# Kernel tuning notes

Measured on AMD Instinct MI355X. Metric: run time of the kernel, lower is better.

The kernel has to match this reference:

```python
import jax, jax.numpy as jnp
import numpy as np

EPS = 1e-8  # torch.nn.CosineSimilarity default eps

def setup_inputs() -> dict:
    key = jax.random.key(0)
    k1, k2 = jax.random.split(key)
    B, R, T, D = 256, 36, 64, 1024
    img_feats = jax.random.normal(k1, (B, R, D), dtype=jnp.float32)
    cap_feats = jax.random.normal(k2, (B, T, D), dtype=jnp.float32)
    cap_mask = jnp.ones((B, T), dtype=jnp.float32)  # unused by the original forward
    return {"img_feats": img_feats, "cap_feats": cap_feats, "cap_mask": cap_mask}

def reference(img_feats, cap_feats, cap_mask):
    # img_feats: (B, R, D); cap_feats: (B, T, D)
    # cosine similarity between every region r and every caption word t:
    # scores[b, r, t] = (img[b,r] . cap[b,t]) / max(||img[b,r]|| * ||cap[b,t]||, eps)
    dots = jnp.einsum('brd,btd->brt', img_feats, cap_feats)
    img_norm = jnp.linalg.norm(img_feats, axis=-1)  # (B, R)
    cap_norm = jnp.linalg.norm(cap_feats, axis=-1)  # (B, T)
    denom = jnp.maximum(img_norm[:, :, None] * cap_norm[:, None, :], EPS)
    scores = dots / denom  # (B, R, T)
    # softmax over regions (dim=1 in the original)
    attn = jax.nn.softmax(scores, axis=1)  # (B, R, T)
    # weighted sum over regions -> per-word image representation (B, T, D)
    img_cap_reps = jnp.einsum('brt,brd->btd', attn, img_feats)
    return img_cap_reps
```

## Files before the change

### kernel.cpp

```cpp
#include <hip/hip_runtime.h>

#define RREG 36
#define TTOK 64
#define DDIM 1024

typedef __attribute__((ext_vector_type(4))) float f32x4;
typedef __attribute__((ext_vector_type(8))) short bf16x8;

__device__ __forceinline__ unsigned short f2bf(float x) {
  unsigned int u = __float_as_uint(x);
  u += 0x7fffu + ((u >> 16) & 1u);
  return (unsigned short)(u >> 16);
}

__global__ __launch_bounds__(1024) void scan_fused(
    const float* __restrict__ img, const float* __restrict__ cap,
    float* __restrict__ out) {
  __shared__ __align__(16) unsigned char smem[52032];

  unsigned short* scap  = (unsigned short*)(smem + 0);
  unsigned short* simg  = (unsigned short*)(smem + 17408);
  unsigned short* simgT = (unsigned short*)(smem + 0);
  float* ssc            = (float*)(smem + 32768);
  unsigned short* satt  = (unsigned short*)(smem + 45440);
  float* sni            = (float*)(smem + 51584);
  float* snc            = (float*)(smem + 51776);

  const int tid  = threadIdx.x;
  const int lane = tid & 63;
  const int wave = tid >> 6;
  const int fm   = lane & 15;
  const int kq   = lane >> 4;
  const int b    = blockIdx.x;

  const float* imgb = img + (size_t)b * RREG * DDIM;
  const float* capb = cap + (size_t)b * TTOK * DDIM;
  float*       outb = out + (size_t)b * TTOK * DDIM;

  const int mt = wave >> 2;
  const int nt = wave & 3;

  f32x4 acc = {0.f, 0.f, 0.f, 0.f};
  float cn0 = 0.f, cn1 = 0.f, in0 = 0.f, in1 = 0.f;

  const int trow = tid >> 5;
  const int d4   = tid & 31;

  for (int c = 0; c < 8; ++c) {
    const int dbase = c * 128 + d4 * 4;
    {
      float4 v = *(const float4*)(capb + trow * DDIM + dbase);
      cn0 += v.x * v.x + v.y * v.y + v.z * v.z + v.w * v.w;
      ushort4 p; p.x = f2bf(v.x); p.y = f2bf(v.y); p.z = f2bf(v.z); p.w = f2bf(v.w);
      *(ushort4*)(scap + trow * 136 + d4 * 4) = p;

      float4 w = *(const float4*)(capb + (trow + 32) * DDIM + dbase);
      cn1 += w.x * w.x + w.y * w.y + w.z * w.z + w.w * w.w;
      ushort4 q; q.x = f2bf(w.x); q.y = f2bf(w.y); q.z = f2bf(w.z); q.w = f2bf(w.w);
      *(ushort4*)(scap + (trow + 32) * 136 + d4 * 4) = q;
    }
    {
      float4 v = *(const float4*)(imgb + trow * DDIM + dbase);
      in0 += v.x * v.x + v.y * v.y + v.z * v.z + v.w * v.w;
      ushort4 p; p.x = f2bf(v.x); p.y = f2bf(v.y); p.z = f2bf(v.z); p.w = f2bf(v.w);
      *(ushort4*)(simg + trow * 136 + d4 * 4) = p;
      if (tid < 512) {
        int r2 = trow + 32;
        float4 w = make_float4(0.f, 0.f, 0.f, 0.f);
        if (r2 < RREG) {
          w = *(const float4*)(imgb + r2 * DDIM + dbase);
          in1 += w.x * w.x + w.y * w.y + w.z * w.z + w.w * w.w;
        }
        ushort4 q; q.x = f2bf(w.x); q.y = f2bf(w.y); q.z = f2bf(w.z); q.w = f2bf(w.w);
        *(ushort4*)(simg + r2 * 136 + d4 * 4) = q;
      }
    }
    __syncthreads();
    if (wave < 12) {
      const unsigned short* arow = simg + (mt * 16 + fm) * 136 + kq * 8;
      const unsigned short* brow = scap + (nt * 16 + fm) * 136 + kq * 8;
#pragma unroll
      for (int ks = 0; ks < 4; ++ks) {
        bf16x8 av = *(const bf16x8*)(arow + ks * 32);
        bf16x8 bv = *(const bf16x8*)(brow + ks * 32);
        acc = __builtin_amdgcn_mfma_f32_16x16x32_bf16(av, bv, acc, 0, 0, 0);
      }
    }
    __syncthreads();
  }

  if (wave < 12) {
#pragma unroll
    for (int i = 0; i < 4; ++i)
      ssc[(mt * 16 + kq * 4 + i) * 66 + nt * 16 + fm] = acc[i];
  }
#pragma unroll
  for (int off = 16; off > 0; off >>= 1) {
    cn0 += __shfl_down(cn0, off, 32);
    cn1 += __shfl_down(cn1, off, 32);
    in0 += __shfl_down(in0, off, 32);
    in1 += __shfl_down(in1, off, 32);
  }
  if ((tid & 31) == 0) {
    snc[trow]      = sqrtf(cn0);
    snc[trow + 32] = sqrtf(cn1);
    sni[trow]      = sqrtf(in0);
    if (trow < 16) sni[trow + 32] = sqrtf(in1);
  }
  __syncthreads();

  if (wave == 0) {
    float cn = snc[lane];
    float s[RREG];
    float mx = -1e30f;
#pragma unroll
    for (int r = 0; r < RREG; ++r) {
      float denom = fmaxf(sni[r] * cn, 1e-8f);
      float v = ssc[r * 66 + lane] / denom;
      s[r] = v;
      mx = fmaxf(mx, v);
    }
    float sum = 0.f;
#pragma unroll
    for (int r = 0; r < RREG; ++r) { float e = __expf(s[r] - mx); s[r] = e; sum += e; }
    float rinv = 1.f / sum;
    unsigned short* ap = satt + lane * 48;
#pragma unroll
    for (int r = 0; r < RREG; ++r) ap[r] = f2bf(s[r] * rinv);
#pragma unroll
    for (int r = RREG; r < 48; ++r) ap[r] = 0;
  }
  __syncthreads();

  const int mtB = wave >> 2;
  const unsigned short* arowB = satt + (mtB * 16 + fm) * 48;
  bf16x8 a1 = *(const bf16x8*)(arowB + kq * 8);
  bf16x8 a2 = {0, 0, 0, 0, 0, 0, 0, 0};
  if (kq < 2) a2 = *(const bf16x8*)(arowB + 32 + kq * 8);

  for (int cb = 0; cb < 8; ++cb) {
    __syncthreads();
    for (int f = tid; f < 1536; f += 1024) {
      int g = f & 511;
      int r = (f >> 9) * 16 + (g & 15);
      int qd = (g >> 4) & 3;
      int sd = g >> 6;
      int dloc = (qd + 4 * sd) * 4;
      float4 v = make_float4(0.f, 0.f, 0.f, 0.f);
      if (r < RREG) v = *(const float4*)(imgb + r * DDIM + cb * 128 + dloc);
      simgT[(dloc + 0) * 56 + r] = f2bf(v.x);
      simgT[(dloc + 1) * 56 + r] = f2bf(v.y);
      simgT[(dloc + 2) * 56 + r] = f2bf(v.z);
      simgT[(dloc + 3) * 56 + r] = f2bf(v.w);
    }
    __syncthreads();
#pragma unroll
    for (int j = 0; j < 2; ++j) {
      int ntB = (wave & 3) * 2 + j;
      const unsigned short* brow = simgT + (ntB * 16 + fm) * 56;
      bf16x8 b1 = *(const bf16x8*)(brow + kq * 8);
      bf16x8 b2 = {0, 0, 0, 0, 0, 0, 0, 0};
      if (kq < 2) b2 = *(const bf16x8*)(brow + 32 + kq * 8);
      f32x4 o = {0.f, 0.f, 0.f, 0.f};
      o = __builtin_amdgcn_mfma_f32_16x16x32_bf16(a1, b1, o, 0, 0, 0);
      o = __builtin_amdgcn_mfma_f32_16x16x32_bf16(a2, b2, o, 0, 0, 0);
#pragma unroll
      for (int i = 0; i < 4; ++i)
        outb[(mtB * 16 + kq * 4 + i) * DDIM + cb * 128 + ntB * 16 + fm] = o[i];
    }
  }
}

extern "C" void kernel_launch(void* const* d_in, const int* in_sizes, int n_in,
                              void* d_out, int out_size, void* d_ws, size_t ws_size,
                              hipStream_t stream) {
  const float* img = (const float*)d_in[0];
  const float* cap = (const float*)d_in[1];
  float* out = (float*)d_out;
  scan_fused<<<dim3(256), dim3(1024), 0, stream>>>(img, cap, out);
}
```

Measured before the change: 159.0 us.

## Split tokens across two blocks and register-prefetch global loads

Each batch now spans two 512-thread blocks, each handling 32 caption tokens, so the grid grows from 256 to 512 blocks and uses smaller LDS for higher occupancy. Both the score GEMM and the weighted-sum loops prefetch the next chunk's global loads into registers before converting and storing the current chunk, which overlaps memory latency with compute. Barriers become a lightweight lgkmcnt wait plus s_barrier, and the block index is swizzled to a different batch/half mapping. The cost is that each image tile is loaded and its norms computed twice, once per token half.

```diff
diff --git a/kernel.cpp b/kernel.cpp
--- a/kernel.cpp
+++ b/kernel.cpp
@@ -3,6 +3,7 @@
 #define RREG 36
 #define TTOK 64
 #define DDIM 1024
+#define TH   32
 
 typedef __attribute__((ext_vector_type(4))) float f32x4;
 typedef __attribute__((ext_vector_type(8))) short bf16x8;
@@ -13,70 +14,95 @@
   return (unsigned short)(u >> 16);
 }
 
-__global__ __launch_bounds__(1024) void scan_fused(
+__device__ __forceinline__ void lds_barrier() {
+  asm volatile("s_waitcnt lgkmcnt(0)" ::: "memory");
+  __builtin_amdgcn_s_barrier();
+}
+
+__global__ __launch_bounds__(512, 4) void scan_fused(
     const float* __restrict__ img, const float* __restrict__ cap,
     float* __restrict__ out) {
-  __shared__ __align__(16) unsigned char smem[52032];
+  __shared__ __align__(16) unsigned char smem[31680];
 
   unsigned short* scap  = (unsigned short*)(smem + 0);
-  unsigned short* simg  = (unsigned short*)(smem + 17408);
+  unsigned short* simg  = (unsigned short*)(smem + 8704);
   unsigned short* simgT = (unsigned short*)(smem + 0);
-  float* ssc            = (float*)(smem + 32768);
-  unsigned short* satt  = (unsigned short*)(smem + 45440);
-  float* sni            = (float*)(smem + 51584);
-  float* snc            = (float*)(smem + 51776);
+  float* ssc            = (float*)(smem + 21760);
+  unsigned short* satt  = (unsigned short*)(smem + 28288);
+  float* sni            = (float*)(smem + 31360);
+  float* snc            = (float*)(smem + 31552);
 
   const int tid  = threadIdx.x;
   const int lane = tid & 63;
   const int wave = tid >> 6;
   const int fm   = lane & 15;
   const int kq   = lane >> 4;
-  const int b    = blockIdx.x;
+
+  const int i     = blockIdx.x;
+  const int b     = ((i & 7) << 5) + (i >> 4);
+  const int tbase = ((i >> 3) & 1) * TH;
 
   const float* imgb = img + (size_t)b * RREG * DDIM;
-  const float* capb = cap + (size_t)b * TTOK * DDIM;
-  float*       outb = out + (size_t)b * TTOK * DDIM;
-
-  const int mt = wave >> 2;
-  const int nt = wave & 3;
-
-  f32x4 acc = {0.f, 0.f, 0.f, 0.f};
-  float cn0 = 0.f, cn1 = 0.f, in0 = 0.f, in1 = 0.f;
+  const float* capb = cap + ((size_t)b * TTOK + tbase) * DDIM;
+  float*       outb = out + ((size_t)b * TTOK + tbase) * DDIM;
 
   const int trow = tid >> 5;
   const int d4   = tid & 31;
 
+  const int mt = wave >> 1;
+  const int nt = wave & 1;
+
+  f32x4 acc = {0.f, 0.f, 0.f, 0.f};
+  float cn0 = 0.f, cn1 = 0.f, in0 = 0.f, in1 = 0.f, in2 = 0.f;
+
+  float4 pc0, pc1, pi0, pi1, pi2;
+  {
+    const float* cp = capb + d4 * 4;
+    const float* ip = imgb + d4 * 4;
+    pc0 = *(const float4*)(cp + trow * DDIM);
+    pc1 = *(const float4*)(cp + (trow + 16) * DDIM);
+    pi0 = *(const float4*)(ip + trow * DDIM);
+    pi1 = *(const float4*)(ip + (trow + 16) * DDIM);
+    pi2 = make_float4(0.f, 0.f, 0.f, 0.f);
+    if (trow < RREG - 32) pi2 = *(const float4*)(ip + (trow + 32) * DDIM);
+  }
+
+#pragma unroll
   for (int c = 0; c < 8; ++c) {
-    const int dbase = c * 128 + d4 * 4;
+    float4 nc0, nc1, ni0, ni1, ni2;
+    if (c < 7) {
+      const float* cp = capb + (c + 1) * 128 + d4 * 4;
+      const float* ip = imgb + (c + 1) * 128 + d4 * 4;
+      nc0 = *(const float4*)(cp + trow * DDIM);
+      nc1 = *(const float4*)(cp + (trow + 16) * DDIM);
+      ni0 = *(const float4*)(ip + trow * DDIM);
+      ni1 = *(const float4*)(ip + (trow + 16) * DDIM);
+      ni2 = make_float4(0.f, 0.f, 0.f, 0.f);
+      if (trow < RREG - 32) ni2 = *(const float4*)(ip + (trow + 32) * DDIM);
+    }
     {
-      float4 v = *(const float4*)(capb + trow * DDIM + dbase);
-      cn0 += v.x * v.x + v.y * v.y + v.z * v.z + v.w * v.w;
-      ushort4 p; p.x = f2bf(v.x); p.y = f2bf(v.y); p.z = f2bf(v.z); p.w = f2bf(v.w);
+      cn0 += pc0.x * pc0.x + pc0.y * pc0.y + pc0.z * pc0.z + pc0.w * pc0.w;
+      ushort4 p; p.x = f2bf(pc0.x); p.y = f2bf(pc0.y); p.z = f2bf(pc0.z); p.w = f2bf(pc0.w);
       *(ushort4*)(scap + trow * 136 + d4 * 4) = p;
 
-      float4 w = *(const float4*)(capb + (trow + 32) * DDIM + dbase);
-      cn1 += w.x * w.x + w.y * w.y + w.z * w.z + w.w * w.w;
-      ushort4 q; q.x = f2bf(w.x); q.y = f2bf(w.y); q.z = f2bf(w.z); q.w = f2bf(w.w);
-      *(ushort4*)(scap + (trow + 32) * 136 + d4 * 4) = q;
-    }
-    {
-      float4 v = *(const float4*)(imgb + trow * DDIM + dbase);
-      in0 += v.x * v.x + v.y * v.y + v.z * v.z + v.w * v.w;
-      ushort4 p; p.x = f2bf(v.x); p.y = f2bf(v.y); p.z = f2bf(v.z); p.w = f2bf(v.w);
-      *(ushort4*)(simg + trow * 136 + d4 * 4) = p;
-      if (tid < 512) {
-        int r2 = trow + 32;
-        float4 w = make_float4(0.f, 0.f, 0.f, 0.f);
-        if (r2 < RREG) {
-          w = *(const float4*)(imgb + r2 * DDIM + dbase);
-          in1 += w.x * w.x + w.y * w.y + w.z * w.z + w.w * w.w;
-        }
-        ushort4 q; q.x = f2bf(w.x); q.y = f2bf(w.y); q.z = f2bf(w.z); q.w = f2bf(w.w);
-        *(ushort4*)(simg + r2 * 136 + d4 * 4) = q;
-      }
-    }
-    __syncthreads();
-    if (wave < 12) {
+      cn1 += pc1.x * pc1.x + pc1.y * pc1.y + pc1.z * pc1.z + pc1.w * pc1.w;
+      ushort4 q; q.x = f2bf(pc1.x); q.y = f2bf(pc1.y); q.z = f2bf(pc1.z); q.w = f2bf(pc1.w);
+      *(ushort4*)(scap + (trow + 16) * 136 + d4 * 4) = q;
+
+      in0 += pi0.x * pi0.x + pi0.y * pi0.y + pi0.z * pi0.z + pi0.w * pi0.w;
+      ushort4 r0; r0.x = f2bf(pi0.x); r0.y = f2bf(pi0.y); r0.z = f2bf(pi0.z); r0.w = f2bf(pi0.w);
+      *(ushort4*)(simg + trow * 136 + d4 * 4) = r0;
+
+      in1 += pi1.x * pi1.x + pi1.y * pi1.y + pi1.z * pi1.z + pi1.w * pi1.w;
+      ushort4 r1; r1.x = f2bf(pi1.x); r1.y = f2bf(pi1.y); r1.z = f2bf(pi1.z); r1.w = f2bf(pi1.w);
+      *(ushort4*)(simg + (trow + 16) * 136 + d4 * 4) = r1;
+
+      in2 += pi2.x * pi2.x + pi2.y * pi2.y + pi2.z * pi2.z + pi2.w * pi2.w;
+      ushort4 r2; r2.x = f2bf(pi2.x); r2.y = f2bf(pi2.y); r2.z = f2bf(pi2.z); r2.w = f2bf(pi2.w);
+      *(ushort4*)(simg + (trow + 32) * 136 + d4 * 4) = r2;
+    }
+    lds_barrier();
+    if (wave < 6) {
       const unsigned short* arow = simg + (mt * 16 + fm) * 136 + kq * 8;
       const unsigned short* brow = scap + (nt * 16 + fm) * 136 + kq * 8;
 #pragma unroll
@@ -86,13 +112,14 @@
         acc = __builtin_amdgcn_mfma_f32_16x16x32_bf16(av, bv, acc, 0, 0, 0);
       }
     }
-    __syncthreads();
-  }
-
-  if (wave < 12) {
-#pragma unroll
-    for (int i = 0; i < 4; ++i)
-      ssc[(mt * 16 + kq * 4 + i) * 66 + nt * 16 + fm] = acc[i];
+    lds_barrier();
+    if (c < 7) { pc0 = nc0; pc1 = nc1; pi0 = ni0; pi1 = ni1; pi2 = ni2; }
+  }
+
+  if (wave < 6) {
+#pragma unroll
+    for (int ii = 0; ii < 4; ++ii)
+      ssc[(mt * 16 + kq * 4 + ii) * 34 + nt * 16 + fm] = acc[ii];
   }
 #pragma unroll
   for (int off = 16; off > 0; off >>= 1) {
@@ -100,23 +127,25 @@
     cn1 += __shfl_down(cn1, off, 32);
     in0 += __shfl_down(in0, off, 32);
     in1 += __shfl_down(in1, off, 32);
+    in2 += __shfl_down(in2, off, 32);
   }
   if ((tid & 31) == 0) {
     snc[trow]      = sqrtf(cn0);
-    snc[trow + 32] = sqrtf(cn1);
+    snc[trow + 16] = sqrtf(cn1);
     sni[trow]      = sqrtf(in0);
-    if (trow < 16) sni[trow + 32] = sqrtf(in1);
-  }
-  __syncthreads();
-
-  if (wave == 0) {
+    sni[trow + 16] = sqrtf(in1);
+    if (trow < RREG - 32) sni[trow + 32] = sqrtf(in2);
+  }
+  lds_barrier();
+
+  if (wave == 0 && lane < TH) {
     float cn = snc[lane];
     float s[RREG];
     float mx = -1e30f;
 #pragma unroll
     for (int r = 0; r < RREG; ++r) {
       float denom = fmaxf(sni[r] * cn, 1e-8f);
-      float v = ssc[r * 66 + lane] / denom;
+      float v = ssc[r * 34 + lane] / denom;
       s[r] = v;
       mx = fmaxf(mx, v);
     }
@@ -130,7 +159,7 @@
 #pragma unroll
     for (int r = RREG; r < 48; ++r) ap[r] = 0;
   }
-  __syncthreads();
+  lds_barrier();
 
   const int mtB = wave >> 2;
   const unsigned short* arowB = satt + (mtB * 16 + fm) * 48;
@@ -138,25 +167,47 @@
   bf16x8 a2 = {0, 0, 0, 0, 0, 0, 0, 0};
   if (kq < 2) a2 = *(const bf16x8*)(arowB + 32 + kq * 8);
 
+  const int rB0  = tid & 15;
+  const int dloc = (((tid >> 4) & 3) + 4 * (tid >> 6)) * 4;
+
+  float4 q0, q1, q2;
+  {
+    const float* ip = imgb + dloc;
+    q0 = *(const float4*)(ip + rB0 * DDIM);
+    q1 = *(const float4*)(ip + (rB0 + 16) * DDIM);
+    q2 = make_float4(0.f, 0.f, 0.f, 0.f);
+    if (rB0 + 32 < RREG) q2 = *(const float4*)(ip + (rB0 + 32) * DDIM);
+  }
+
+#pragma unroll
   for (int cb = 0; cb < 8; ++cb) {
-    __syncthreads();
-    for (int f = tid; f < 1536; f += 1024) {
-      int g = f & 511;
-      int r = (f >> 9) * 16 + (g & 15);
-      int qd = (g >> 4) & 3;
-      int sd = g >> 6;
-      int dloc = (qd + 4 * sd) * 4;
-      float4 v = make_float4(0.f, 0.f, 0.f, 0.f);
-      if (r < RREG) v = *(const float4*)(imgb + r * DDIM + cb * 128 + dloc);
-      simgT[(dloc + 0) * 56 + r] = f2bf(v.x);
-      simgT[(dloc + 1) * 56 + r] = f2bf(v.y);
-      simgT[(dloc + 2) * 56 + r] = f2bf(v.z);
-      simgT[(dloc + 3) * 56 + r] = f2bf(v.w);
-    }
-    __syncthreads();
+    float4 n0, n1, n2;
+    if (cb < 7) {
+      const float* ip = imgb + (cb + 1) * 128 + dloc;
+      n0 = *(const float4*)(ip + rB0 * DDIM);
+      n1 = *(const float4*)(ip + (rB0 + 16) * DDIM);
+      n2 = make_float4(0.f, 0.f, 0.f, 0.f);
+      if (rB0 + 32 < RREG) n2 = *(const float4*)(ip + (rB0 + 32) * DDIM);
+    }
+    {
+      unsigned short* tp = simgT + dloc * 56;
+      tp[0 * 56 + rB0] = f2bf(q0.x);
+      tp[1 * 56 + rB0] = f2bf(q0.y);
+      tp[2 * 56 + rB0] = f2bf(q0.z);
+      tp[3 * 56 + rB0] = f2bf(q0.w);
+      tp[0 * 56 + rB0 + 16] = f2bf(q1.x);
+      tp[1 * 56 + rB0 + 16] = f2bf(q1.y);
+      tp[2 * 56 + rB0 + 16] = f2bf(q1.z);
+      tp[3 * 56 + rB0 + 16] = f2bf(q1.w);
+      tp[0 * 56 + rB0 + 32] = f2bf(q2.x);
+      tp[1 * 56 + rB0 + 32] = f2bf(q2.y);
+      tp[2 * 56 + rB0 + 32] = f2bf(q2.z);
+      tp[3 * 56 + rB0 + 32] = f2bf(q2.w);
+    }
+    lds_barrier();
 #pragma unroll
     for (int j = 0; j < 2; ++j) {
-      int ntB = (wave & 3) * 2 + j;
+      const int ntB = (wave & 3) * 2 + j;
       const unsigned short* brow = simgT + (ntB * 16 + fm) * 56;
       bf16x8 b1 = *(const bf16x8*)(brow + kq * 8);
       bf16x8 b2 = {0, 0, 0, 0, 0, 0, 0, 0};
@@ -165,8 +216,12 @@
       o = __builtin_amdgcn_mfma_f32_16x16x32_bf16(a1, b1, o, 0, 0, 0);
       o = __builtin_amdgcn_mfma_f32_16x16x32_bf16(a2, b2, o, 0, 0, 0);
 #pragma unroll
-      for (int i = 0; i < 4; ++i)
-        outb[(mtB * 16 + kq * 4 + i) * DDIM + cb * 128 + ntB * 16 + fm] = o[i];
+      for (int ii = 0; ii < 4; ++ii)
+        outb[(mtB * 16 + kq * 4 + ii) * DDIM + cb * 128 + ntB * 16 + fm] = o[ii];
+    }
+    if (cb < 7) {
+      lds_barrier();
+      q0 = n0; q1 = n1; q2 = n2;
     }
   }
 }
@@ -177,5 +232,5 @@
   const float* img = (const float*)d_in[0];
   const float* cap = (const float*)d_in[1];
   float* out = (float*)d_out;
-  scan_fused<<<dim3(256), dim3(1024), 0, stream>>>(img, cap, out);
-}
+  scan_fused<<<dim3(512), dim3(512), 0, stream>>>(img, cap, out);
+}
```

After: 200.1 us. +25.8%, slower.

## Double-buffer LDS staging with register prefetch across both GEMM phases

Applied to the files above, without the earlier changes.

Turns both GEMM phases into a software pipeline. Global loads for chunk c+2 are issued ahead while chunk c+1 is converted into the other LDS buffer and chunk c is consumed by MFMA, so each iteration needs one barrier instead of two. The first image-transpose chunks for phase two are prefetched during the tail of phase one. Barriers become a bare s_waitcnt lgkmcnt plus s_barrier, and launch bounds add a min-blocks hint. This costs more LDS and more live registers, which may hurt occupancy at 1024 threads.

```diff
diff --git a/kernel.cpp b/kernel.cpp
--- a/kernel.cpp
+++ b/kernel.cpp
@@ -13,18 +13,20 @@
   return (unsigned short)(u >> 16);
 }
 
-__global__ __launch_bounds__(1024) void scan_fused(
+__device__ __forceinline__ void lds_barrier() {
+  asm volatile("s_waitcnt lgkmcnt(0)" ::: "memory");
+  __builtin_amdgcn_s_barrier();
+}
+
+__global__ __launch_bounds__(1024, 4) void scan_fused(
     const float* __restrict__ img, const float* __restrict__ cap,
     float* __restrict__ out) {
-  __shared__ __align__(16) unsigned char smem[52032];
-
-  unsigned short* scap  = (unsigned short*)(smem + 0);
-  unsigned short* simg  = (unsigned short*)(smem + 17408);
-  unsigned short* simgT = (unsigned short*)(smem + 0);
-  float* ssc            = (float*)(smem + 32768);
-  unsigned short* satt  = (unsigned short*)(smem + 45440);
-  float* sni            = (float*)(smem + 51584);
-  float* snc            = (float*)(smem + 51776);
+  __shared__ __align__(16) unsigned char smem[60928];
+
+  float* ssc            = (float*)(smem + 30464);
+  unsigned short* satt  = (unsigned short*)(smem + 43136);
+  float* sni            = (float*)(smem + 49280);
+  float* snc            = (float*)(smem + 49472);
 
   const int tid  = threadIdx.x;
   const int lane = tid & 63;
@@ -37,48 +39,55 @@
   const float* capb = cap + (size_t)b * TTOK * DDIM;
   float*       outb = out + (size_t)b * TTOK * DDIM;
 
-  const int mt = wave >> 2;
-  const int nt = wave & 3;
+  const int trow = tid >> 5;
+  const int d4   = tid & 31;
+  const int mt   = wave >> 2;
+  const int nt   = wave & 3;
+
+  const int rB   = ((tid >> 9) << 4) | (tid & 15);
+  const int gB   = tid & 511;
+  const int dlB  = ((((gB >> 4) & 3) + ((gB >> 6) << 2)) << 2);
+  const bool hasB2 = (tid < 512);
+  const int rB2  = 32 + (tid & 15);
 
   f32x4 acc = {0.f, 0.f, 0.f, 0.f};
   float cn0 = 0.f, cn1 = 0.f, in0 = 0.f, in1 = 0.f;
 
-  const int trow = tid >> 5;
-  const int d4   = tid & 31;
-
-  for (int c = 0; c < 8; ++c) {
-    const int dbase = c * 128 + d4 * 4;
-    {
-      float4 v = *(const float4*)(capb + trow * DDIM + dbase);
-      cn0 += v.x * v.x + v.y * v.y + v.z * v.z + v.w * v.w;
-      ushort4 p; p.x = f2bf(v.x); p.y = f2bf(v.y); p.z = f2bf(v.z); p.w = f2bf(v.w);
-      *(ushort4*)(scap + trow * 136 + d4 * 4) = p;
-
-      float4 w = *(const float4*)(capb + (trow + 32) * DDIM + dbase);
-      cn1 += w.x * w.x + w.y * w.y + w.z * w.z + w.w * w.w;
-      ushort4 q; q.x = f2bf(w.x); q.y = f2bf(w.y); q.z = f2bf(w.z); q.w = f2bf(w.w);
-      *(ushort4*)(scap + (trow + 32) * 136 + d4 * 4) = q;
-    }
-    {
-      float4 v = *(const float4*)(imgb + trow * DDIM + dbase);
-      in0 += v.x * v.x + v.y * v.y + v.z * v.z + v.w * v.w;
-      ushort4 p; p.x = f2bf(v.x); p.y = f2bf(v.y); p.z = f2bf(v.z); p.w = f2bf(v.w);
-      *(ushort4*)(simg + trow * 136 + d4 * 4) = p;
-      if (tid < 512) {
-        int r2 = trow + 32;
-        float4 w = make_float4(0.f, 0.f, 0.f, 0.f);
-        if (r2 < RREG) {
-          w = *(const float4*)(imgb + r2 * DDIM + dbase);
-          in1 += w.x * w.x + w.y * w.y + w.z * w.z + w.w * w.w;
-        }
-        ushort4 q; q.x = f2bf(w.x); q.y = f2bf(w.y); q.z = f2bf(w.z); q.w = f2bf(w.w);
-        *(ushort4*)(simg + r2 * 136 + d4 * 4) = q;
-      }
-    }
-    __syncthreads();
+  auto issueA = [&](int c, float4& c0v, float4& c1v, float4& i0v, float4& i1v) {
+    const float* cp = capb + c * 128 + d4 * 4;
+    const float* ip = imgb + c * 128 + d4 * 4;
+    c0v = *(const float4*)(cp + trow * DDIM);
+    c1v = *(const float4*)(cp + (trow + 32) * DDIM);
+    i0v = *(const float4*)(ip + trow * DDIM);
+    i1v = make_float4(0.f, 0.f, 0.f, 0.f);
+    if (tid < 512 && trow + 32 < RREG)
+      i1v = *(const float4*)(ip + (trow + 32) * DDIM);
+  };
+  auto stageA = [&](int par, const float4& c0v, const float4& c1v,
+                    const float4& i0v, const float4& i1v) {
+    unsigned short* sc = (unsigned short*)(smem + par * 30464);
+    unsigned short* si = sc + 8704;
+    cn0 += c0v.x * c0v.x + c0v.y * c0v.y + c0v.z * c0v.z + c0v.w * c0v.w;
+    ushort4 p; p.x = f2bf(c0v.x); p.y = f2bf(c0v.y); p.z = f2bf(c0v.z); p.w = f2bf(c0v.w);
+    *(ushort4*)(sc + trow * 136 + d4 * 4) = p;
+    cn1 += c1v.x * c1v.x + c1v.y * c1v.y + c1v.z * c1v.z + c1v.w * c1v.w;
+    ushort4 q; q.x = f2bf(c1v.x); q.y = f2bf(c1v.y); q.z = f2bf(c1v.z); q.w = f2bf(c1v.w);
+    *(ushort4*)(sc + (trow + 32) * 136 + d4 * 4) = q;
+    in0 += i0v.x * i0v.x + i0v.y * i0v.y + i0v.z * i0v.z + i0v.w * i0v.w;
+    ushort4 r0; r0.x = f2bf(i0v.x); r0.y = f2bf(i0v.y); r0.z = f2bf(i0v.z); r0.w = f2bf(i0v.w);
+    *(ushort4*)(si + trow * 136 + d4 * 4) = r0;
+    if (tid < 512) {
+      in1 += i1v.x * i1v.x + i1v.y * i1v.y + i1v.z * i1v.z + i1v.w * i1v.w;
+      ushort4 r1; r1.x = f2bf(i1v.x); r1.y = f2bf(i1v.y); r1.z = f2bf(i1v.z); r1.w = f2bf(i1v.w);
+      *(ushort4*)(si + (trow + 32) * 136 + d4 * 4) = r1;
+    }
+  };
+  auto mfmaA = [&](int par) {
     if (wave < 12) {
-      const unsigned short* arow = simg + (mt * 16 + fm) * 136 + kq * 8;
-      const unsigned short* brow = scap + (nt * 16 + fm) * 136 + kq * 8;
+      const unsigned short* sc = (const unsigned short*)(smem + par * 30464);
+      const unsigned short* si = sc + 8704;
+      const unsigned short* arow = si + (mt * 16 + fm) * 136 + kq * 8;
+      const unsigned short* brow = sc + (nt * 16 + fm) * 136 + kq * 8;
 #pragma unroll
       for (int ks = 0; ks < 4; ++ks) {
         bf16x8 av = *(const bf16x8*)(arow + ks * 32);
@@ -86,13 +95,52 @@
         acc = __builtin_amdgcn_mfma_f32_16x16x32_bf16(av, bv, acc, 0, 0, 0);
       }
     }
-    __syncthreads();
+  };
+  auto issueB = [&](int cb, float4& q0, float4& q1) {
+    const float* ip = imgb + cb * 128 + dlB;
+    q0 = *(const float4*)(ip + rB * DDIM);
+    q1 = make_float4(0.f, 0.f, 0.f, 0.f);
+    if (hasB2 && rB2 < RREG) q1 = *(const float4*)(ip + rB2 * DDIM);
+  };
+  auto stageB = [&](int par, const float4& q0, const float4& q1) {
+    unsigned short* tp = (unsigned short*)(smem + par * 14336) + dlB * 56;
+    tp[0 * 56 + rB] = f2bf(q0.x);
+    tp[1 * 56 + rB] = f2bf(q0.y);
+    tp[2 * 56 + rB] = f2bf(q0.z);
+    tp[3 * 56 + rB] = f2bf(q0.w);
+    if (hasB2) {
+      tp[0 * 56 + rB2] = f2bf(q1.x);
+      tp[1 * 56 + rB2] = f2bf(q1.y);
+      tp[2 * 56 + rB2] = f2bf(q1.z);
+      tp[3 * 56 + rB2] = f2bf(q1.w);
+    }
+  };
+
+  float4 tc0, tc1, ti0, ti1;
+  float4 cc0, cc1, ci0, ci1;
+  float4 nc0, nc1, ni0, ni1;
+  float4 bq0a, bq0b, bq1a, bq1b;
+
+  issueA(0, tc0, tc1, ti0, ti1);
+  issueA(1, cc0, cc1, ci0, ci1);
+  stageA(0, tc0, tc1, ti0, ti1);
+  lds_barrier();
+
+  for (int c = 0; c < 8; ++c) {
+    if (c < 6)        issueA(c + 2, nc0, nc1, ni0, ni1);
+    else if (c == 6)  issueB(0, bq0a, bq0b);
+    else              issueB(1, bq1a, bq1b);
+    if (c < 7)        stageA((c + 1) & 1, cc0, cc1, ci0, ci1);
+    else              stageB(0, bq0a, bq0b);
+    mfmaA(c & 1);
+    lds_barrier();
+    cc0 = nc0; cc1 = nc1; ci0 = ni0; ci1 = ni1;
   }
 
   if (wave < 12) {
 #pragma unroll
-    for (int i = 0; i < 4; ++i)
-      ssc[(mt * 16 + kq * 4 + i) * 66 + nt * 16 + fm] = acc[i];
+    for (int i2 = 0; i2 < 4; ++i2)
+      ssc[(mt * 16 + kq * 4 + i2) * 66 + nt * 16 + fm] = acc[i2];
   }
 #pragma unroll
   for (int off = 16; off > 0; off >>= 1) {
@@ -107,7 +155,7 @@
     sni[trow]      = sqrtf(in0);
     if (trow < 16) sni[trow + 32] = sqrtf(in1);
   }
-  __syncthreads();
+  lds_barrier();
 
   if (wave == 0) {
     float cn = snc[lane];
@@ -130,7 +178,7 @@
 #pragma unroll
     for (int r = RREG; r < 48; ++r) ap[r] = 0;
   }
-  __syncthreads();
+  lds_barrier();
 
   const int mtB = wave >> 2;
   const unsigned short* arowB = satt + (mtB * 16 + fm) * 48;
@@ -138,36 +186,31 @@
   bf16x8 a2 = {0, 0, 0, 0, 0, 0, 0, 0};
   if (kq < 2) a2 = *(const bf16x8*)(arowB + 32 + kq * 8);
 
+  float4 pq0 = bq1a, pq1 = bq1b;
+  float4 nq0, nq1;
+
   for (int cb = 0; cb < 8; ++cb) {
-    __syncthreads();
-    for (int f = tid; f < 1536; f += 1024) {
-      int g = f & 511;
-      int r = (f >> 9) * 16 + (g & 15);
-      int qd = (g >> 4) & 3;
-      int sd = g >> 6;
-      int dloc = (qd + 4 * sd) * 4;
-      float4 v = make_float4(0.f, 0.f, 0.f, 0.f);
-      if (r < RREG) v = *(const float4*)(imgb + r * DDIM + cb * 128 + dloc);
-      simgT[(dloc + 0) * 56 + r] = f2bf(v.x);
-      simgT[(dloc + 1) * 56 + r] = f2bf(v.y);
-      simgT[(dloc + 2) * 56 + r] = f2bf(v.z);
-      simgT[(dloc + 3) * 56 + r] = f2bf(v.w);
-    }
-    __syncthreads();
-#pragma unroll
-    for (int j = 0; j < 2; ++j) {
-      int ntB = (wave & 3) * 2 + j;
-      const unsigned short* brow = simgT + (ntB * 16 + fm) * 56;
-      bf16x8 b1 = *(const bf16x8*)(brow + kq * 8);
-      bf16x8 b2 = {0, 0, 0, 0, 0, 0, 0, 0};
-      if (kq < 2) b2 = *(const bf16x8*)(brow + 32 + kq * 8);
-      f32x4 o = {0.f, 0.f, 0.f, 0.f};
-      o = __builtin_amdgcn_mfma_f32_16x16x32_bf16(a1, b1, o, 0, 0, 0);
-      o = __builtin_amdgcn_mfma_f32_16x16x32_bf16(a2, b2, o, 0, 0, 0);
-#pragma unroll
-      for (int i = 0; i < 4; ++i)
-        outb[(mtB * 16 + kq * 4 + i) * DDIM + cb * 128 + ntB * 16 + fm] = o[i];
-    }
+    if (cb < 6) issueB(cb + 2, nq0, nq1);
+    if (cb < 7) stageB((cb + 1) & 1, pq0, pq1);
+    {
+      const unsigned short* st = (const unsigned short*)(smem + (cb & 1) * 14336);
+#pragma unroll
+      for (int j = 0; j < 2; ++j) {
+        const int ntB = (wave & 3) * 2 + j;
+        const unsigned short* brow = st + (ntB * 16 + fm) * 56;
+        bf16x8 b1 = *(const bf16x8*)(brow + kq * 8);
+        bf16x8 b2 = {0, 0, 0, 0, 0, 0, 0, 0};
+        if (kq < 2) b2 = *(const bf16x8*)(brow + 32 + kq * 8);
+        f32x4 o = {0.f, 0.f, 0.f, 0.f};
+        o = __builtin_amdgcn_mfma_f32_16x16x32_bf16(a1, b1, o, 0, 0, 0);
+        o = __builtin_amdgcn_mfma_f32_16x16x32_bf16(a2, b2, o, 0, 0, 0);
+#pragma unroll
+        for (int i2 = 0; i2 < 4; ++i2)
+          outb[(mtB * 16 + kq * 4 + i2) * DDIM + cb * 128 + ntB * 16 + fm] = o[i2];
+      }
+    }
+    lds_barrier();
+    pq0 = nq0; pq1 = nq1;
   }
 }
 
```

Measured after the change: 163.1 us. 1.03x slower.

## Load GEMM operands directly from global into registers, dropping LDS staging

Applied to the files above, without the earlier changes.

Both matrix-multiply phases now read their MFMA operand fragments straight from global memory into registers and convert them to bf16 in place. This removes the shared-memory staging buffers and the block-wide barriers inside each chunk loop. Norms are computed from the same register loads and reduced with cross-lane shuffles. The trade is redundant global reads (each image and caption row is fetched by several waves) and strided, less coalesced column loads in the second GEMM, in exchange for much lower LDS use and less synchronisation. The launch-bounds hint is also raised to request more resident blocks.

```diff
diff --git a/kernel.cpp b/kernel.cpp
--- a/kernel.cpp
+++ b/kernel.cpp
@@ -13,18 +13,22 @@
   return (unsigned short)(u >> 16);
 }
 
-__global__ __launch_bounds__(1024) void scan_fused(
+__device__ __forceinline__ bf16x8 cvt8(float4 a, float4 b) {
+  bf16x8 r;
+  r[0] = (short)f2bf(a.x); r[1] = (short)f2bf(a.y);
+  r[2] = (short)f2bf(a.z); r[3] = (short)f2bf(a.w);
+  r[4] = (short)f2bf(b.x); r[5] = (short)f2bf(b.y);
+  r[6] = (short)f2bf(b.z); r[7] = (short)f2bf(b.w);
+  return r;
+}
+
+__global__ __launch_bounds__(1024, 4) void scan_fused(
     const float* __restrict__ img, const float* __restrict__ cap,
     float* __restrict__ out) {
-  __shared__ __align__(16) unsigned char smem[52032];
-
-  unsigned short* scap  = (unsigned short*)(smem + 0);
-  unsigned short* simg  = (unsigned short*)(smem + 17408);
-  unsigned short* simgT = (unsigned short*)(smem + 0);
-  float* ssc            = (float*)(smem + 32768);
-  unsigned short* satt  = (unsigned short*)(smem + 45440);
-  float* sni            = (float*)(smem + 51584);
-  float* snc            = (float*)(smem + 51776);
+  __shared__ __align__(16) float ssc[48 * 66];
+  __shared__ __align__(16) unsigned short satt[64 * 48];
+  __shared__ float sni[48];
+  __shared__ float snc[TTOK];
 
   const int tid  = threadIdx.x;
   const int lane = tid & 63;
@@ -37,75 +41,51 @@
   const float* capb = cap + (size_t)b * TTOK * DDIM;
   float*       outb = out + (size_t)b * TTOK * DDIM;
 
-  const int mt = wave >> 2;
-  const int nt = wave & 3;
+  if (wave < 12) {
+    const int mt = wave >> 2;
+    const int nt = wave & 3;
+    const int ar = mt * 16 + fm;
+    const int br = nt * 16 + fm;
+    const bool avld = (ar < RREG);
+    const float* ap = imgb + (size_t)ar * DDIM + kq * 8;
+    const float* bp = capb + (size_t)br * DDIM + kq * 8;
 
-  f32x4 acc = {0.f, 0.f, 0.f, 0.f};
-  float cn0 = 0.f, cn1 = 0.f, in0 = 0.f, in1 = 0.f;
+    f32x4 acc = {0.f, 0.f, 0.f, 0.f};
+    float nI = 0.f, nC = 0.f;
+    const float4 z4 = make_float4(0.f, 0.f, 0.f, 0.f);
 
-  const int trow = tid >> 5;
-  const int d4   = tid & 31;
-
-  for (int c = 0; c < 8; ++c) {
-    const int dbase = c * 128 + d4 * 4;
-    {
-      float4 v = *(const float4*)(capb + trow * DDIM + dbase);
-      cn0 += v.x * v.x + v.y * v.y + v.z * v.z + v.w * v.w;
-      ushort4 p; p.x = f2bf(v.x); p.y = f2bf(v.y); p.z = f2bf(v.z); p.w = f2bf(v.w);
-      *(ushort4*)(scap + trow * 136 + d4 * 4) = p;
-
-      float4 w = *(const float4*)(capb + (trow + 32) * DDIM + dbase);
-      cn1 += w.x * w.x + w.y * w.y + w.z * w.z + w.w * w.w;
-      ushort4 q; q.x = f2bf(w.x); q.y = f2bf(w.y); q.z = f2bf(w.z); q.w = f2bf(w.w);
-      *(ushort4*)(scap + (trow + 32) * 136 + d4 * 4) = q;
-    }
-    {
-      float4 v = *(const float4*)(imgb + trow * DDIM + dbase);
-      in0 += v.x * v.x + v.y * v.y + v.z * v.z + v.w * v.w;
-      ushort4 p; p.x = f2bf(v.x); p.y = f2bf(v.y); p.z = f2bf(v.z); p.w = f2bf(v.w);
-      *(ushort4*)(simg + trow * 136 + d4 * 4) = p;
-      if (tid < 512) {
-        int r2 = trow + 32;
-        float4 w = make_float4(0.f, 0.f, 0.f, 0.f);
-        if (r2 < RREG) {
-          w = *(const float4*)(imgb + r2 * DDIM + dbase);
-          in1 += w.x * w.x + w.y * w.y + w.z * w.z + w.w * w.w;
-        }
-        ushort4 q; q.x = f2bf(w.x); q.y = f2bf(w.y); q.z = f2bf(w.z); q.w = f2bf(w.w);
-        *(ushort4*)(simg + r2 * 136 + d4 * 4) = q;
+    for (int c = 0; c < 8; ++c) {
+      float4 A0[4], A1[4], B0[4], B1[4];
+#pragma unroll
+      for (int ks = 0; ks < 4; ++ks) {
+        const float* a = ap + c * 128 + ks * 32;
+        const float* q = bp + c * 128 + ks * 32;
+        A0[ks] = avld ? *(const float4*)(a)     : z4;
+        A1[ks] = avld ? *(const float4*)(a + 4) : z4;
+        B0[ks] = *(const float4*)(q);
+        B1[ks] = *(const float4*)(q + 4);
+      }
+#pragma unroll
+      for (int ks = 0; ks < 4; ++ks) {
+        nI += A0[ks].x * A0[ks].x + A0[ks].y * A0[ks].y +
+              A0[ks].z * A0[ks].z + A0[ks].w * A0[ks].w +
+              A1[ks].x * A1[ks].x + A1[ks].y * A1[ks].y +
+              A1[ks].z * A1[ks].z + A1[ks].w * A1[ks].w;
+        nC += B0[ks].x * B0[ks].x + B0[ks].y * B0[ks].y +
+              B0[ks].z * B0[ks].z + B0[ks].w * B0[ks].w +
+              B1[ks].x * B1[ks].x + B1[ks].y * B1[ks].y +
+              B1[ks].z * B1[ks].z + B1[ks].w * B1[ks].w;
+        acc = __builtin_amdgcn_mfma_f32_16x16x32_bf16(
+            cvt8(A0[ks], A1[ks]), cvt8(B0[ks], B1[ks]), acc, 0, 0, 0);
       }
     }
-    __syncthreads();
-    if (wave < 12) {
-      const unsigned short* arow = simg + (mt * 16 + fm) * 136 + kq * 8;
-      const unsigned short* brow = scap + (nt * 16 + fm) * 136 + kq * 8;
-#pragma unroll
-      for (int ks = 0; ks < 4; ++ks) {
-        bf16x8 av = *(const bf16x8*)(arow + ks * 32);
-        bf16x8 bv = *(const bf16x8*)(brow + ks * 32);
-        acc = __builtin_amdgcn_mfma_f32_16x16x32_bf16(av, bv, acc, 0, 0, 0);
-      }
-    }
-    __syncthreads();
-  }
-
-  if (wave < 12) {
 #pragma unroll
     for (int i = 0; i < 4; ++i)
       ssc[(mt * 16 + kq * 4 + i) * 66 + nt * 16 + fm] = acc[i];
-  }
-#pragma unroll
-  for (int off = 16; off > 0; off >>= 1) {
-    cn0 += __shfl_down(cn0, off, 32);
-    cn1 += __shfl_down(cn1, off, 32);
-    in0 += __shfl_down(in0, off, 32);
-    in1 += __shfl_down(in1, off, 32);
-  }
-  if ((tid & 31) == 0) {
-    snc[trow]      = sqrtf(cn0);
-    snc[trow + 32] = sqrtf(cn1);
-    sni[trow]      = sqrtf(in0);
-    if (trow < 16) sni[trow + 32] = sqrtf(in1);
+    nI += __shfl_xor(nI, 16); nI += __shfl_xor(nI, 32);
+    nC += __shfl_xor(nC, 16); nC += __shfl_xor(nC, 32);
+    if (nt == 0 && kq == 0 && avld) sni[ar] = sqrtf(nI);
+    if (mt == 0 && kq == 0)         snc[br] = sqrtf(nC);
   }
   __syncthreads();
 
@@ -124,11 +104,11 @@
 #pragma unroll
     for (int r = 0; r < RREG; ++r) { float e = __expf(s[r] - mx); s[r] = e; sum += e; }
     float rinv = 1.f / sum;
-    unsigned short* ap = satt + lane * 48;
+    unsigned short* ap2 = satt + lane * 48;
 #pragma unroll
-    for (int r = 0; r < RREG; ++r) ap[r] = f2bf(s[r] * rinv);
+    for (int r = 0; r < RREG; ++r) ap2[r] = f2bf(s[r] * rinv);
 #pragma unroll
-    for (int r = RREG; r < 48; ++r) ap[r] = 0;
+    for (int r = RREG; r < 48; ++r) ap2[r] = 0;
   }
   __syncthreads();
 
@@ -139,34 +119,28 @@
   if (kq < 2) a2 = *(const bf16x8*)(arowB + 32 + kq * 8);
 
   for (int cb = 0; cb < 8; ++cb) {
-    __syncthreads();
-    for (int f = tid; f < 1536; f += 1024) {
-      int g = f & 511;
-      int r = (f >> 9) * 16 + (g & 15);
-      int qd = (g >> 4) & 3;
-      int sd = g >> 6;
-      int dloc = (qd + 4 * sd) * 4;
-      float4 v = make_float4(0.f, 0.f, 0.f, 0.f);
-      if (r < RREG) v = *(const float4*)(imgb + r * DDIM + cb * 128 + dloc);
-      simgT[(dloc + 0) * 56 + r] = f2bf(v.x);
-      simgT[(dloc + 1) * 56 + r] = f2bf(v.y);
-      simgT[(dloc + 2) * 56 + r] = f2bf(v.z);
-      simgT[(dloc + 3) * 56 + r] = f2bf(v.w);
-    }
-    __syncthreads();
 #pragma unroll
     for (int j = 0; j < 2; ++j) {
-      int ntB = (wave & 3) * 2 + j;
-      const unsigned short* brow = simgT + (ntB * 16 + fm) * 56;
-      bf16x8 b1 = *(const bf16x8*)(brow + kq * 8);
+      const int d = cb * 128 + ((wave & 3) * 2 + j) * 16 + fm;
+      const float* cp = imgb + d;
+      float bvx[8];
+#pragma unroll
+      for (int r = 0; r < 8; ++r)
+        bvx[r] = cp[(size_t)(kq * 8 + r) * DDIM];
+      bf16x8 b1;
+#pragma unroll
+      for (int r = 0; r < 8; ++r) b1[r] = (short)f2bf(bvx[r]);
       bf16x8 b2 = {0, 0, 0, 0, 0, 0, 0, 0};
-      if (kq < 2) b2 = *(const bf16x8*)(brow + 32 + kq * 8);
+      if (kq == 0) {
+#pragma unroll
+        for (int r = 0; r < 4; ++r) b2[r] = (short)f2bf(cp[(size_t)(32 + r) * DDIM]);
+      }
       f32x4 o = {0.f, 0.f, 0.f, 0.f};
       o = __builtin_amdgcn_mfma_f32_16x16x32_bf16(a1, b1, o, 0, 0, 0);
       o = __builtin_amdgcn_mfma_f32_16x16x32_bf16(a2, b2, o, 0, 0, 0);
 #pragma unroll
       for (int i = 0; i < 4; ++i)
-        outb[(mtB * 16 + kq * 4 + i) * DDIM + cb * 128 + ntB * 16 + fm] = o[i];
+        outb[(size_t)(mtB * 16 + kq * 4 + i) * DDIM + d] = o[i];
     }
   }
 }
```

Result: slower. 216.7 us (+36.2%).
